# Kernel tuning notes

Measured on AMD Instinct MI355X. Metric: run time of the kernel, lower is better.

## Reference

```python
import jax, jax.numpy as jnp
import numpy as np
from jax import lax

DN = ('NCHW', 'OIHW', 'NCHW')

def _conv(x, w, b):
    # stride-2 conv, kernel 4, padding 1 (PyTorch Conv2d semantics)
    y = lax.conv_general_dilated(x, w, (2, 2), [(1, 1), (1, 1)], dimension_numbers=DN)
    return y + b[None, :, None, None]

def _deconv(x, w, b):
    # PyTorch ConvTranspose2d(k=4, stride=2, padding=1): conv with lhs_dilation=2,
    # padding k-1-p=2, kernel rot180 with in/out axes swapped ([I,O,H,W] -> [O,I,H,W])
    k = jnp.transpose(jnp.flip(w, (2, 3)), (1, 0, 2, 3))
    y = lax.conv_general_dilated(x, k, (1, 1), [(2, 2), (2, 2)], lhs_dilation=(2, 2),
                                 dimension_numbers=DN)
    return y + b[None, :, None, None]

def setup_inputs() -> dict:
    key = jax.random.key(0)
    ks = jax.random.split(key, 16)
    K, D = 1024, 2048
    s = lambda *sh: 0.05
    inp = {
        'x': jax.random.uniform(ks[0], (8, 3, 256, 256), jnp.float32),
        'enc_w1': jax.random.normal(ks[1], (128, 3, 4, 4), jnp.float32) * 0.05,
        'enc_b1': jnp.zeros((128,), jnp.float32),
        'enc_w2': jax.random.normal(ks[2], (128, 128, 4, 4), jnp.float32) * 0.02,
        'enc_b2': jnp.zeros((128,), jnp.float32),
        'enc_w3': jax.random.normal(ks[3], (D, 128, 4, 4), jnp.float32) * 0.02,
        'enc_b3': jnp.zeros((D,), jnp.float32),
        'codebook': jax.random.uniform(ks[4], (K, D), jnp.float32, -1.0 / K, 1.0 / K),
        'dec_w1': jax.random.normal(ks[5], (D, 128, 4, 4), jnp.float32) * 0.02,  # [in,out,kH,kW]
        'dec_b1': jnp.zeros((128,), jnp.float32),
        'dec_w2': jax.random.normal(ks[6], (128, 128, 4, 4), jnp.float32) * 0.02,
        'dec_b2': jnp.zeros((128,), jnp.float32),
        'dec_w3': jax.random.normal(ks[7], (128, 1, 4, 4), jnp.float32) * 0.05,
        'dec_b3': jnp.zeros((1,), jnp.float32),
    }
    return inp

def reference(x, enc_w1, enc_b1, enc_w2, enc_b2, enc_w3, enc_b3, codebook,
              dec_w1, dec_b1, dec_w2, dec_b2, dec_w3, dec_b3):
    # encoder
    h = jax.nn.relu(_conv(x, enc_w1, enc_b1))
    h = jax.nn.relu(_conv(h, enc_w2, enc_b2))
    z_e = _conv(h, enc_w3, enc_b3)                       # [B, D, H8, W8]
    B, D, Hq, Wq = z_e.shape
    z_flat = z_e.reshape(B, D, Hq * Wq).transpose(0, 2, 1)  # [B, N, D]
    # squared distances to codebook [K, D]
    dists = (jnp.sum(z_flat ** 2, axis=2, keepdims=True)
             + jnp.sum(codebook ** 2, axis=1)
             - 2.0 * jnp.einsum('bnd,kd->bnk', z_flat, codebook))  # [B, N, K]
    idx = jnp.argmin(dists, axis=2)                      # [B, N]
    z_q = codebook[idx]                                  # [B, N, D]
    z_q = z_q.transpose(0, 2, 1).reshape(B, D, Hq, Wq)
    # decoder
    h = jax.nn.relu(_deconv(z_q, dec_w1, dec_b1))
    h = jax.nn.relu(_deconv(h, dec_w2, dec_b2))
    x_recon = jax.nn.sigmoid(_deconv(h, dec_w3, dec_b3))  # [B, 1, H, W]
    sg = lax.stop_gradient
    commitment = 0.25 * jnp.mean((sg(z_e) - z_q) ** 2)
    quantization = jnp.mean((z_e - sg(z_q)) ** 2)
    return x_recon, commitment + quantization
```

## Files before the change

### kernel.cpp

```cpp
#include <hip/hip_runtime.h>

typedef __attribute__((ext_vector_type(8))) short bf16x8;
typedef __attribute__((ext_vector_type(4))) float f32x4;

__device__ __forceinline__ unsigned short f2bf(float f) {
  unsigned u = __float_as_uint(f);
  u += 0x7fff + ((u >> 16) & 1);
  return (unsigned short)(u >> 16);
}
__device__ __forceinline__ float bf2f(unsigned short h) {
  return __uint_as_float(((unsigned)h) << 16);
}

__device__ __forceinline__ void gload_lds16(const void* g, void* l) {
  __builtin_amdgcn_global_load_lds((const __attribute__((address_space(1))) void*)g,
                                   (__attribute__((address_space(3))) void*)l, 16, 0, 0);
}

__device__ __forceinline__ void pbar() {
  asm volatile("" ::: "memory");
  __builtin_amdgcn_sched_barrier(0);
  __builtin_amdgcn_s_barrier();
  __builtin_amdgcn_sched_barrier(0);
  asm volatile("" ::: "memory");
}


__global__ __launch_bounds__(256) void pack_conv_w(const float* __restrict__ w,
                                                   unsigned short* __restrict__ bt,
                                                   int Cin, int total) {
  int i = blockIdx.x * 256 + threadIdx.x;
  if (i >= total) return;
  int ci = i % Cin;
  int kk = (i / Cin) % 16;
  int co = i / (Cin * 16);
  bt[i] = f2bf(w[(size_t)co * Cin * 16 + (size_t)ci * 16 + kk]);
}

__global__ __launch_bounds__(256) void pack_deconv_w(const float* __restrict__ w,
                                                     unsigned short* __restrict__ btd,
                                                     int Cin, int total) {
  int i = blockIdx.x * 256 + threadIdx.x;
  if (i >= total) return;
  int ci = i % Cin;
  int t = (i / Cin) & 3;
  int co = (i / (Cin * 4)) & 127;
  int z = i / (Cin * 4 * 128);
  int py = z >> 1, px = z & 1;
  int ty = t >> 1, tx = t & 1;
  int ky = 2 * ty + 1 - py, kx = 2 * tx + 1 - px;
  btd[i] = f2bf(w[(((size_t)ci * 128 + co) * 4 + ky) * 4 + kx]);
}

__global__ __launch_bounds__(256) void pack_w1v(const float* __restrict__ w,
                                                unsigned short* __restrict__ bt) {
  int i = blockIdx.x * 256 + threadIdx.x;
  int ci = i & 2047;
  int n = i >> 11;
  int co = n & 127;
  int t = n >> 7;
  bt[i] = f2bf(w[(((size_t)ci * 128 + co) << 4) + t]);
}

__global__ __launch_bounds__(256) void pack_w3(const float* __restrict__ w3,
                                               float* __restrict__ wd) {
  int i = blockIdx.x * 256 + threadIdx.x;
  int ci = i & 127;
  int t = (i >> 7) & 3;
  int z = i >> 9;
  int py = z >> 1, px = z & 1, ty = t >> 1, tx = t & 1;
  int ky = 2 * ty + 1 - py, kx = 2 * tx + 1 - px;
  wd[i] = w3[ci * 16 + ky * 4 + kx];
}

__global__ __launch_bounds__(256) void pack_cb(const float* __restrict__ cb,
                                               unsigned short* __restrict__ cbb,
                                               float* __restrict__ cnorm) {
  int r = blockIdx.x;
  const float* src = cb + (size_t)r * 2048;
  float s = 0.f;
  for (int i = threadIdx.x; i < 2048; i += 256) {
    float v = src[i];
    cbb[(size_t)r * 2048 + i] = f2bf(v);
    s += v * v;
  }
  __shared__ float red[4];
  for (int off = 32; off > 0; off >>= 1) s += __shfl_down(s, off, 64);
  int lane = threadIdx.x & 63, wid = threadIdx.x >> 6;
  if (lane == 0) red[wid] = s;
  __syncthreads();
  if (threadIdx.x == 0) cnorm[r] = red[0] + red[1] + red[2] + red[3];
}

__global__ __launch_bounds__(256) void conv1_k(const float* __restrict__ x,
                                               const float* __restrict__ w1,
                                               const float* __restrict__ b1,
                                               unsigned short* __restrict__ h1) {
  __shared__ float sIn[3][4][258];
  int b = blockIdx.x >> 7, y = blockIdx.x & 127;
  for (int i = threadIdx.x; i < 3 * 4 * 258; i += 256) {
    int c = i / (4 * 258);
    int rr = (i / 258) % 4;
    int col = i % 258;
    int iy = 2 * y - 1 + rr;
    int ix = col - 1;
    float v = (iy >= 0 && iy < 256 && ix >= 0 && ix < 256)
                  ? x[((size_t)(b * 3 + c) * 256 + iy) * 256 + ix] : 0.f;
    sIn[c][rr][col] = v;
  }
  __syncthreads();
  int co = threadIdx.x & 127, xh = threadIdx.x >> 7;
  float w[3][4][4];
#pragma unroll
  for (int c = 0; c < 3; ++c)
#pragma unroll
    for (int ky = 0; ky < 4; ++ky)
#pragma unroll
      for (int kx = 0; kx < 4; ++kx)
        w[c][ky][kx] = w1[(((size_t)co * 3 + c) * 4 + ky) * 4 + kx];
  float bb = b1[co];
  for (int xi = 0; xi < 64; ++xi) {
    int xx = xh * 64 + xi;
    float acc = bb;
#pragma unroll
    for (int c = 0; c < 3; ++c)
#pragma unroll
      for (int ky = 0; ky < 4; ++ky)
#pragma unroll
        for (int kx = 0; kx < 4; ++kx)
          acc += sIn[c][ky][2 * xx + kx] * w[c][ky][kx];
    acc = acc > 0.f ? acc : 0.f;
    h1[((size_t)(b * 130 + y + 1) * 130 + (xx + 1)) * 128 + co] = f2bf(acc);
  }
}

#define GM_CONV 0
#define GM_DECONV 1
#define GM_FLAT 2
#define EP_PM 0
#define EP_FLATBF 1
#define EP_F32 2

struct GP {
  const unsigned short* A;
  const unsigned short* Bt;
  const float* bias;
  void* out;
  int Klen, Clog;
  int MXlog, MYlog;
  int WPin, strideBA;
  int HPo, WPo;
  int Nout;
  int BrowStride;
  int BclassStride;
  int classLog;
  int TPC;
  int outZ;
};

template <int BM, int GM, int EP, int RELU>
__global__ __launch_bounds__(256) void gemm_k(GP p) {
  constexpr int MFR = BM / 32;
  constexpr int CA = BM / 32;
  const int tid = threadIdx.x;
  const int lane = tid & 63;
  const int wid = tid >> 6;
  const int m0 = blockIdx.x * BM;
  const int n0 = blockIdx.y * 128;
  const int zAll = blockIdx.z;
  const int zc = zAll & ((1 << p.classLog) - 1);
  const int chunk = zAll >> p.classLog;
  const int py = zc >> 1, px = zc & 1;

  __shared__ __align__(16) unsigned short sA[BM * 64];
  __shared__ __align__(16) unsigned short sB[128 * 64];

  const unsigned short* Bt = p.Bt + (size_t)zc * p.BclassStride;
  const int C = 1 << p.Clog;
  const int tb = chunk * p.TPC;
  const int chunkOff = tb << p.Clog;
  const int sw = ((lane & 7) ^ (lane >> 3)) * 8;

  int rcA[CA];
#pragma unroll
  for (int i = 0; i < CA; ++i) {
    int r = (wid * CA + i) * 8 + (lane >> 3);
    int m = m0 + r;
    if (GM == GM_FLAT) {
      rcA[i] = m * p.Klen;
    } else {
      int mx = m & ((1 << p.MXlog) - 1);
      int my = (m >> p.MXlog) & ((1 << p.MYlog) - 1);
      int b = m >> (p.MXlog + p.MYlog);
      if (GM == GM_CONV)
        rcA[i] = b * p.strideBA + ((2 * my) * p.WPin + 2 * mx) * C;
      else
        rcA[i] = b * p.strideBA + ((my + 1) * p.WPin + (mx + 1)) * C;
    }
  }
  int rcB[4];
#pragma unroll
  for (int i = 0; i < 4; ++i) {
    int r = (wid * 4 + i) * 8 + (lane >> 3);
    rcB[i] = (n0 + r) * p.BrowStride;
  }

  f32x4 acc[MFR][4];
#pragma unroll
  for (int a = 0; a < MFR; ++a)
#pragma unroll
    for (int b = 0; b < 4; ++b) acc[a][b] = (f32x4){0.f, 0.f, 0.f, 0.f};

  const int nsteps = p.Klen >> 6;
  for (int ks = 0; ks < nsteps; ++ks) {
    const int k0 = ks << 6;
    int tap = 0;
    if (GM == GM_CONV) {
      int t = tb + (k0 >> p.Clog);
      tap = ((t >> 2) * p.WPin + (t & 3)) * C;
    } else if (GM == GM_DECONV) {
      int t = tb + (k0 >> p.Clog);
      int ty = t >> 1, tx = t & 1;
      tap = ((py - ty) * p.WPin + (px - tx)) * C;
    }
    const int ci0 = k0 & (C - 1);
    const int aoff = tap + ci0 + sw;
#pragma unroll
    for (int i = 0; i < CA; ++i)
      gload_lds16(p.A + rcA[i] + aoff, &sA[(wid * CA + i) * 512]);
#pragma unroll
    for (int i = 0; i < 4; ++i)
      gload_lds16(Bt + rcB[i] + chunkOff + k0 + sw, &sB[(wid * 4 + i) * 512]);
    __syncthreads();

#pragma unroll
    for (int kk = 0; kk < 2; ++kk) {
      bf16x8 af[MFR], bfv[4];
#pragma unroll
      for (int mf = 0; mf < MFR; ++mf) {
        int row = (wid >> 1) * (BM / 2) + mf * 16 + (lane & 15);
        int col = (kk * 64 + ((lane >> 4) << 4)) ^ ((row & 7) << 4);
        af[mf] = *(const bf16x8*)((const char*)sA + row * 128 + col);
      }
#pragma unroll
      for (int nf = 0; nf < 4; ++nf) {
        int row = (wid & 1) * 64 + nf * 16 + (lane & 15);
        int col = (kk * 64 + ((lane >> 4) << 4)) ^ ((row & 7) << 4);
        bfv[nf] = *(const bf16x8*)((const char*)sB + row * 128 + col);
      }
#pragma unroll
      for (int mf = 0; mf < MFR; ++mf)
#pragma unroll
        for (int nf = 0; nf < 4; ++nf)
          acc[mf][nf] = __builtin_amdgcn_mfma_f32_16x16x32_bf16(
              af[mf], bfv[nf], acc[mf][nf], 0, 0, 0);
    }
    __syncthreads();
  }

  const int wr = wid >> 1, wc = wid & 1;
#pragma unroll
  for (int mf = 0; mf < MFR; ++mf) {
#pragma unroll
    for (int j = 0; j < 4; ++j) {
      int row = m0 + wr * (BM / 2) + mf * 16 + ((lane >> 4) << 2) + j;
      int b = 0, my = 0, mx = 0;
      if (EP == EP_PM) {
        mx = row & ((1 << p.MXlog) - 1);
        my = (row >> p.MXlog) & ((1 << p.MYlog) - 1);
        b = row >> (p.MXlog + p.MYlog);
      }
#pragma unroll
      for (int nf = 0; nf < 4; ++nf) {
        int col = n0 + wc * 64 + nf * 16 + (lane & 15);
        float v = acc[mf][nf][j];
        if (EP == EP_PM || EP == EP_FLATBF) v += p.bias[col];
        if (RELU) v = v > 0.f ? v : 0.f;
        if (EP == EP_F32) {
          ((float*)p.out)[(size_t)row * p.Nout + col] = v;
        } else if (EP == EP_FLATBF) {
          ((unsigned short*)p.out)[(size_t)row * p.Nout + col] = f2bf(v);
        } else {
          int oy, ox;
          if (GM == GM_DECONV) {
            oy = 2 * my + py + 1;
            ox = 2 * mx + px + 1;
          } else {
            oy = my + 1;
            ox = mx + 1;
          }
          ((unsigned short*)p.out)[((size_t)(b * p.HPo + oy) * p.WPo + ox) * 128 + col] =
              f2bf(v);
        }
      }
    }
  }
}

struct G2 {
  const unsigned short* A;
  const unsigned short* Bt;
  const float* bias;
  unsigned short* out;
  int Klen;
  int WPin, strideBA;
  int Nout;
};

template <int GM>
__global__ __launch_bounds__(512, 2) void gemm256_k(G2 p) {
  __shared__ __align__(16) unsigned short lds[8 * 8192];
  const int tid = threadIdx.x, lane = tid & 63, wid = tid >> 6;
  const int wr = wid >> 2, wc = wid & 3;
  const int m0 = blockIdx.x * 256, n0 = blockIdx.y * 256;
  const int sw = ((lane & 7) ^ (lane >> 3)) * 8;
  const int xc0 = ((lane >> 4) ^ (lane & 7)) * 16;
  const int xc1 = (((lane >> 4) | 4) ^ (lane & 7)) * 16;

  int rcA[2][2], rcB[2][2];
#pragma unroll
  for (int h = 0; h < 2; ++h)
#pragma unroll
    for (int i = 0; i < 2; ++i) {
      int m = m0 + h * 128 + wid * 16 + i * 8 + (lane >> 3);
      if (GM == GM_CONV) {
        int mx = m & 31, my = (m >> 5) & 31, b = m >> 10;
        rcA[h][i] = b * p.strideBA + ((2 * my) * p.WPin + 2 * mx) * 128;
      } else {
        rcA[h][i] = m * p.Klen;
      }
      int n = n0 + h * 128 + wid * 16 + i * 8 + (lane >> 3);
      rcB[h][i] = n * p.Klen;
    }

  const int JMAX = p.Klen >> 4;

  auto stage = [&](int j) {
    if (j >= JMAX) return;
    const int T = j >> 2, type = j & 3, slot = j & 7;
    unsigned short* dst = &lds[slot * 8192 + wid * 1024];
    if (type < 2) {
      const int ko = (T << 6) + sw;
      gload_lds16(p.Bt + rcB[type][0] + ko, dst);
      gload_lds16(p.Bt + rcB[type][1] + ko, dst + 512);
    } else {
      int ko;
      if (GM == GM_CONV) {
        const int t = T >> 1;
        ko = ((t >> 2) * p.WPin + (t & 3)) * 128 + ((T & 1) << 6) + sw;
      } else {
        ko = (T << 6) + sw;
      }
      gload_lds16(p.A + rcA[type - 2][0] + ko, dst);
      gload_lds16(p.A + rcA[type - 2][1] + ko, dst + 512);
    }
  };

  f32x4 acc[8][4];
#pragma unroll
  for (int i = 0; i < 8; ++i)
#pragma unroll
    for (int j = 0; j < 4; ++j) acc[i][j] = (f32x4){0.f, 0.f, 0.f, 0.f};

#pragma unroll
  for (int j = 0; j < 6; ++j) stage(j);
  asm volatile("s_waitcnt vmcnt(4)" ::: "memory");
  pbar();

  const int NT = p.Klen >> 6;
  bf16x8 a[4][2], b0[2][2], b1[2][2];
  for (int t = 0; t < NT; ++t) {
    const int sb = (t & 1) << 2;
    const char* myA = (const char*)&lds[(sb + 2 + wr) * 8192];
    const char* myB = (const char*)&lds[(sb + (wc >> 1)) * 8192];
    const int p4 = t << 2;
#pragma unroll
    for (int mf = 0; mf < 4; ++mf) {
      const int r = mf * 16 + (lane & 15);
      a[mf][0] = *(const bf16x8*)(myA + r * 128 + xc0);
      a[mf][1] = *(const bf16x8*)(myA + r * 128 + xc1);
    }
#pragma unroll
    for (int nf = 0; nf < 2; ++nf) {
      const int c = (wc & 1) * 64 + nf * 16 + (lane & 15);
      b0[nf][0] = *(const bf16x8*)(myB + c * 128 + xc0);
      b0[nf][1] = *(const bf16x8*)(myB + c * 128 + xc1);
    }
    stage(p4 + 6);
    pbar();
    __builtin_amdgcn_s_setprio(1);
#pragma unroll
    for (int mf = 0; mf < 4; ++mf)
#pragma unroll
      for (int nf = 0; nf < 2; ++nf)
#pragma unroll
        for (int kk = 0; kk < 2; ++kk)
          acc[mf][nf] = __builtin_amdgcn_mfma_f32_16x16x32_bf16(
              a[mf][kk], b0[nf][kk], acc[mf][nf], 0, 0, 0);
    __builtin_amdgcn_s_setprio(0);
    pbar();
#pragma unroll
    for (int nf = 0; nf < 2; ++nf) {
      const int c = (wc & 1) * 64 + (nf + 2) * 16 + (lane & 15);
      b1[nf][0] = *(const bf16x8*)(myB + c * 128 + xc0);
      b1[nf][1] = *(const bf16x8*)(myB + c * 128 + xc1);
    }
    stage(p4 + 7);
    pbar();
    __builtin_amdgcn_s_setprio(1);
#pragma unroll
    for (int mf = 0; mf < 4; ++mf)
#pragma unroll
      for (int nf = 0; nf < 2; ++nf)
#pragma unroll
        for (int kk = 0; kk < 2; ++kk)
          acc[mf][nf + 2] = __builtin_amdgcn_mfma_f32_16x16x32_bf16(
              a[mf][kk], b1[nf][kk], acc[mf][nf + 2], 0, 0, 0);
    __builtin_amdgcn_s_setprio(0);
    pbar();
#pragma unroll
    for (int mf = 0; mf < 4; ++mf) {
      const int r = 64 + mf * 16 + (lane & 15);
      a[mf][0] = *(const bf16x8*)(myA + r * 128 + xc0);
      a[mf][1] = *(const bf16x8*)(myA + r * 128 + xc1);
    }
    stage(p4 + 8);
    pbar();
    __builtin_amdgcn_s_setprio(1);
#pragma unroll
    for (int mf = 0; mf < 4; ++mf)
#pragma unroll
      for (int nf = 0; nf < 2; ++nf)
#pragma unroll
        for (int kk = 0; kk < 2; ++kk)
          acc[mf + 4][nf + 2] = __builtin_amdgcn_mfma_f32_16x16x32_bf16(
              a[mf][kk], b1[nf][kk], acc[mf + 4][nf + 2], 0, 0, 0);
    __builtin_amdgcn_s_setprio(0);
    pbar();
    stage(p4 + 9);
    pbar();
    __builtin_amdgcn_s_setprio(1);
#pragma unroll
    for (int mf = 0; mf < 4; ++mf)
#pragma unroll
      for (int nf = 0; nf < 2; ++nf)
#pragma unroll
        for (int kk = 0; kk < 2; ++kk)
          acc[mf + 4][nf] = __builtin_amdgcn_mfma_f32_16x16x32_bf16(
              a[mf][kk], b0[nf][kk], acc[mf + 4][nf], 0, 0, 0);
    __builtin_amdgcn_s_setprio(0);
    asm volatile("s_waitcnt vmcnt(4)" ::: "memory");
    pbar();
  }

#pragma unroll
  for (int mf = 0; mf < 8; ++mf) {
#pragma unroll
    for (int j = 0; j < 4; ++j) {
      int row = m0 + wr * 128 + mf * 16 + ((lane >> 4) << 2) + j;
#pragma unroll
      for (int nf = 0; nf < 4; ++nf) {
        int col = n0 + wc * 64 + nf * 16 + (lane & 15);
        float v = acc[mf][nf][j] + p.bias[col];
        p.out[(size_t)row * p.Nout + col] = f2bf(v);
      }
    }
  }
}

struct GV {
  const unsigned short* A;
  const unsigned short* Bt;
  const float* cnorm;
  float* cval;
  int* cidx;
};

__global__ __launch_bounds__(512, 2) void vq8_k(GV p) {
  __shared__ __align__(16) unsigned short lds[49152];
  const int tid = threadIdx.x, lane = tid & 63, wid = tid >> 6;
  const int wr = wid >> 2, wc = wid & 3;
  const int m0 = blockIdx.x * 128, n0 = blockIdx.y * 256;
  const int sw = ((lane & 7) ^ (lane >> 3)) * 8;
  const int xc0 = ((lane >> 4) ^ (lane & 7)) * 16;
  const int xc1 = (((lane >> 4) | 4) ^ (lane & 7)) * 16;
  const int K = 2048;

  int rcA[2];
#pragma unroll
  for (int h = 0; h < 2; ++h)
    rcA[h] = (m0 + h * 64 + wid * 8 + (lane >> 3)) * K;
  int rcB[2][2];
#pragma unroll
  for (int h = 0; h < 2; ++h)
#pragma unroll
    for (int i = 0; i < 2; ++i)
      rcB[h][i] = (n0 + h * 128 + wid * 16 + i * 8 + (lane >> 3)) * K;

  auto stage = [&](int j) {
    if (j >= 128) return;
    const int T = j >> 2, type = j & 3;
    unsigned short* reg = &lds[(T & 1) * 24576];
    const int ko = (T << 6) + sw;
    if (type < 2) {
      gload_lds16(p.A + rcA[type] + ko, reg + type * 4096 + wid * 512);
    } else {
      unsigned short* d = reg + 8192 + (type - 2) * 8192 + wid * 1024;
      gload_lds16(p.Bt + rcB[type - 2][0] + ko, d);
      gload_lds16(p.Bt + rcB[type - 2][1] + ko, d + 512);
    }
  };

  f32x4 acc[4][4];
#pragma unroll
  for (int i = 0; i < 4; ++i)
#pragma unroll
    for (int j = 0; j < 4; ++j) acc[i][j] = (f32x4){0.f, 0.f, 0.f, 0.f};

#pragma unroll
  for (int j = 0; j < 6; ++j) stage(j);
  asm volatile("s_waitcnt vmcnt(2)" ::: "memory");
  pbar();

  bf16x8 a[4][2], b[4][2];
  for (int t = 0; t < 32; ++t) {
    const char* reg = (const char*)&lds[(t & 1) * 24576];
    const char* myA = reg + wr * 8192;
    const char* myB = reg + 16384 + (wc >> 1) * 16384;
    const int p4 = t << 2;
#pragma unroll
    for (int mf = 0; mf < 4; ++mf) {
      const int r = mf * 16 + (lane & 15);
      a[mf][0] = *(const bf16x8*)(myA + r * 128 + xc0);
      a[mf][1] = *(const bf16x8*)(myA + r * 128 + xc1);
    }
#pragma unroll
    for (int nf = 0; nf < 4; ++nf) {
      const int c = (wc & 1) * 64 + nf * 16 + (lane & 15);
      b[nf][0] = *(const bf16x8*)(myB + c * 128 + xc0);
      b[nf][1] = *(const bf16x8*)(myB + c * 128 + xc1);
    }
    stage(p4 + 6);
    stage(p4 + 7);
    pbar();
    __builtin_amdgcn_s_setprio(1);
#pragma unroll
    for (int mf = 0; mf < 4; ++mf)
#pragma unroll
      for (int nf = 0; nf < 2; ++nf)
#pragma unroll
        for (int kk = 0; kk < 2; ++kk)
          acc[mf][nf] = __builtin_amdgcn_mfma_f32_16x16x32_bf16(
              a[mf][kk], b[nf][kk], acc[mf][nf], 0, 0, 0);
    __builtin_amdgcn_s_setprio(0);
    pbar();
    stage(p4 + 8);
    stage(p4 + 9);
    pbar();
    __builtin_amdgcn_s_setprio(1);
#pragma unroll
    for (int mf = 0; mf < 4; ++mf)
#pragma unroll
      for (int nf = 2; nf < 4; ++nf)
#pragma unroll
        for (int kk = 0; kk < 2; ++kk)
          acc[mf][nf] = __builtin_amdgcn_mfma_f32_16x16x32_bf16(
              a[mf][kk], b[nf][kk], acc[mf][nf], 0, 0, 0);
    __builtin_amdgcn_s_setprio(0);
    asm volatile("s_waitcnt vmcnt(2)" ::: "memory");
    pbar();
  }

  __syncthreads();
  float* sV = (float*)lds;
  int* sI = (int*)(sV + 512);
  float cn[4];
#pragma unroll
  for (int nf = 0; nf < 4; ++nf)
    cn[nf] = p.cnorm[n0 + wc * 64 + nf * 16 + (lane & 15)];
#pragma unroll
  for (int mf = 0; mf < 4; ++mf) {
#pragma unroll
    for (int j = 0; j < 4; ++j) {
      float bv = 3.4e38f;
      int bi = 0x7fffffff;
#pragma unroll
      for (int nf = 0; nf < 4; ++nf) {
        int col = n0 + wc * 64 + nf * 16 + (lane & 15);
        float d = cn[nf] - 2.f * acc[mf][nf][j];
        if (d < bv) { bv = d; bi = col; }
      }
#pragma unroll
      for (int w = 1; w <= 8; w <<= 1) {
        float ov = __shfl_xor(bv, w, 64);
        int oi = __shfl_xor(bi, w, 64);
        if (ov < bv || (ov == bv && oi < bi)) { bv = ov; bi = oi; }
      }
      int lrow = wr * 64 + mf * 16 + ((lane >> 4) << 2) + j;
      if ((lane & 15) == 0) { sV[lrow * 4 + wc] = bv; sI[lrow * 4 + wc] = bi; }
    }
  }
  __syncthreads();
  if (tid < 128) {
    float bv = sV[tid * 4];
    int bi = sI[tid * 4];
#pragma unroll
    for (int c = 1; c < 4; ++c) {
      float v = sV[tid * 4 + c];
      int i2 = sI[tid * 4 + c];
      if (v < bv) { bv = v; bi = i2; }
    }
    p.cval[(size_t)(m0 + tid) * 4 + blockIdx.y] = bv;
    p.cidx[(size_t)(m0 + tid) * 4 + blockIdx.y] = bi;
  }
}


__global__ __launch_bounds__(256) void argfin_k(const float* __restrict__ cval,
                                                const int* __restrict__ cidx,
                                                int* __restrict__ idx,
                                                float* __restrict__ dmin) {
  int m = blockIdx.x * 256 + threadIdx.x;
  float bv = cval[(size_t)m * 4];
  int bi = cidx[(size_t)m * 4];
#pragma unroll
  for (int j = 1; j < 4; ++j) {
    float v = cval[(size_t)m * 4 + j];
    int i2 = cidx[(size_t)m * 4 + j];
    if (v < bv) { bv = v; bi = i2; }
  }
  idx[m] = bi;
  dmin[m] = bv;
}


__global__ __launch_bounds__(256) void lossz_k(const unsigned short* __restrict__ zf,
                                               const float* __restrict__ dmin,
                                               float* __restrict__ part) {
  int m = blockIdx.x;
  int tid = threadIdx.x;
  bf16x8 av = ((const bf16x8*)(zf + (size_t)m * 2048))[tid];
  float s = 0.f;
#pragma unroll
  for (int i = 0; i < 8; ++i) {
    float z = bf2f((unsigned short)av[i]);
    s += z * z;
  }
  __shared__ float red[4];
  for (int off = 32; off > 0; off >>= 1) s += __shfl_down(s, off, 64);
  int lane = tid & 63, wid = tid >> 6;
  if (lane == 0) red[wid] = s;
  __syncthreads();
  if (tid == 0) part[m] = red[0] + red[1] + red[2] + red[3] + dmin[m];
}

__global__ __launch_bounds__(256) void loss_final_k(const float* __restrict__ part,
                                                    float* __restrict__ out) {
  int tid = threadIdx.x;
  float s = 0.f;
  for (int i = tid; i < 8192; i += 256) s += part[i];
  __shared__ float red[4];
  for (int off = 32; off > 0; off >>= 1) s += __shfl_down(s, off, 64);
  if ((tid & 63) == 0) red[tid >> 6] = s;
  __syncthreads();
  if (tid == 0) out[0] = 1.25f * (red[0] + red[1] + red[2] + red[3]) / 16777216.f;
}

__global__ __launch_bounds__(256) void dc1gather_k(const float* __restrict__ V,
                                                   const int* __restrict__ idx,
                                                   const float* __restrict__ bias,
                                                   unsigned short* __restrict__ h3) {
  int b = blockIdx.x >> 6;
  int oy = blockIdx.x & 63;
  int co = threadIdx.x & 127;
  int xh = threadIdx.x >> 7;
  __shared__ int sIdx[2][32];
  int iyA = (oy + 1) >> 1, kyA = (oy + 1) & 1;
  int iyB = iyA - 1, kyB = kyA + 2;
  if (threadIdx.x < 64) {
    int which = threadIdx.x >> 5;
    int ix = threadIdx.x & 31;
    int iy = which ? iyB : iyA;
    sIdx[which][ix] = (iy >= 0 && iy < 32) ? idx[(b << 10) + (iy << 5) + ix] : -1;
  }
  __syncthreads();
  float bb = bias[co];
  for (int xi = 0; xi < 32; ++xi) {
    int ox = xh * 32 + xi;
    int ixA = (ox + 1) >> 1, kxA = (ox + 1) & 1;
    int ixB = ixA - 1, kxB = kxA + 2;
    float s = bb;
    int kAA = (ixA < 32) ? sIdx[0][ixA] : -1;
    if (kAA >= 0) s += V[((size_t)(kAA * 16 + kyA * 4 + kxA)) * 128 + co];
    int kAB = (ixB >= 0) ? sIdx[0][ixB] : -1;
    if (kAB >= 0) s += V[((size_t)(kAB * 16 + kyA * 4 + kxB)) * 128 + co];
    int kBA = (ixA < 32) ? sIdx[1][ixA] : -1;
    if (kBA >= 0) s += V[((size_t)(kBA * 16 + kyB * 4 + kxA)) * 128 + co];
    int kBB = (ixB >= 0) ? sIdx[1][ixB] : -1;
    if (kBB >= 0) s += V[((size_t)(kBB * 16 + kyB * 4 + kxB)) * 128 + co];
    s = s > 0.f ? s : 0.f;
    h3[((size_t)(b * 66 + oy + 1) * 66 + (ox + 1)) * 128 + co] = f2bf(s);
  }
}

__global__ __launch_bounds__(256) void deconv3_k(const unsigned short* __restrict__ h4,
                                                 const float* __restrict__ wd,
                                                 const float* __restrict__ b3,
                                                 float* __restrict__ out) {
  __shared__ __align__(16) char sRow[2 * 130 * 272];
  __shared__ float sW[2048];
  const int tid = threadIdx.x;
  const int b = blockIdx.x >> 8, oy = blockIdx.x & 255;
  const int py = oy & 1, uy = oy >> 1;
  const int g0 = uy + py;
  for (int i = tid; i < 2048; i += 256) sW[i] = wd[i];
  for (int g = tid; g < 4160; g += 256) {
    int r = (g >= 2080) ? 1 : 0;
    int gg = g - r * 2080;
    int px = gg >> 4, k = gg & 15;
    const bf16x8* src =
        (const bf16x8*)(h4 + (((size_t)(b * 130 + g0 + r) * 130 + px) << 7) + k * 8);
    *(bf16x8*)(sRow + r * 35360 + px * 272 + k * 16) = *src;
  }
  __syncthreads();
  const int ox = tid;
  const int pxp = ox & 1, ux = ox >> 1;
  const int z = py * 2 + pxp;
  float s = b3[0];
#pragma unroll
  for (int ty = 0; ty < 2; ++ty) {
#pragma unroll
    for (int tx = 0; tx < 2; ++tx) {
      int ixp = ux + 1 + pxp - tx;
      const char* base = sRow + (1 - ty) * 35360 + ixp * 272;
      const float* wp = &sW[z * 512 + (ty * 2 + tx) * 128];
#pragma unroll
      for (int k = 0; k < 16; ++k) {
        bf16x8 v = *(const bf16x8*)(base + k * 16);
#pragma unroll
        for (int i = 0; i < 8; ++i)
          s += bf2f((unsigned short)v[i]) * wp[k * 8 + i];
      }
    }
  }
  out[(size_t)blockIdx.x * 256 + ox] = 1.f / (1.f + __expf(-s));
}

extern "C" void kernel_launch(void* const* d_in, const int* in_sizes, int n_in,
                              void* d_out, int out_size, void* d_ws, size_t ws_size,
                              hipStream_t stream) {
  const float* x = (const float*)d_in[0];
  const float* ew1 = (const float*)d_in[1];
  const float* eb1 = (const float*)d_in[2];
  const float* ew2 = (const float*)d_in[3];
  const float* eb2 = (const float*)d_in[4];
  const float* ew3 = (const float*)d_in[5];
  const float* eb3 = (const float*)d_in[6];
  const float* cb = (const float*)d_in[7];
  const float* dw1 = (const float*)d_in[8];
  const float* db1 = (const float*)d_in[9];
  const float* dw2 = (const float*)d_in[10];
  const float* db2 = (const float*)d_in[11];
  const float* dw3 = (const float*)d_in[12];
  const float* db3 = (const float*)d_in[13];
  float* out = (float*)d_out;

  char* w = (char*)d_ws;
  size_t off = 0;
  auto alloc = [&](size_t bytes) {
    char* p = w + off;
    off = (off + bytes + 255) & ~(size_t)255;
    return p;
  };
  const size_t sz_h1 = 8ull * 130 * 130 * 128 * 2;
  const size_t sz_h2 = 8ull * 66 * 66 * 128 * 2;
  const size_t sz_zf = 8192ull * 2048 * 2;
  unsigned short* h1 = (unsigned short*)alloc(sz_h1);
  unsigned short* h2 = (unsigned short*)alloc(sz_h2);
  unsigned short* zf = (unsigned short*)alloc(sz_zf);
  unsigned short* cbb = (unsigned short*)alloc(1024ull * 2048 * 2);
  float* cnorm = (float*)alloc(1024 * 4);
  int* idx = (int*)alloc(8192 * 4);
  unsigned short* h4 = (unsigned short*)alloc(sz_h1);
  unsigned short* bt2 = (unsigned short*)alloc(128ull * 2048 * 2);
  unsigned short* bt3 = (unsigned short*)alloc(2048ull * 2048 * 2);
  unsigned short* btw1 = (unsigned short*)alloc(2048ull * 2048 * 2);
  unsigned short* btd2 = (unsigned short*)alloc(4ull * 128 * 512 * 2);
  float* V = (float*)alloc(1024ull * 16 * 128 * 4);
  float* lpart = (float*)alloc(8192 * 4);
  float* wd3 = (float*)alloc(2048 * 4);
  unsigned short* h3 = (unsigned short*)alloc(sz_h2);
  float* cval = (float*)alloc(8192ull * 4 * 4);
  int* cidx = (int*)alloc(8192ull * 4 * 4);
  float* dmin = (float*)alloc(8192 * 4);

  hipMemsetAsync(h1, 0, sz_h1, stream);
  hipMemsetAsync(h2, 0, sz_h2, stream);
  hipMemsetAsync(h3, 0, sz_h2, stream);
  hipMemsetAsync(h4, 0, sz_h1, stream);

  pack_conv_w<<<(128 * 128 * 16) / 256, 256, 0, stream>>>(ew2, bt2, 128, 128 * 128 * 16);
  pack_conv_w<<<(2048 * 128 * 16) / 256, 256, 0, stream>>>(ew3, bt3, 128, 2048 * 128 * 16);
  pack_w1v<<<(2048 * 2048) / 256, 256, 0, stream>>>(dw1, btw1);
  pack_deconv_w<<<(4 * 128 * 4 * 128) / 256, 256, 0, stream>>>(dw2, btd2, 128, 4 * 128 * 4 * 128);
  pack_w3<<<8, 256, 0, stream>>>(dw3, wd3);
  pack_cb<<<1024, 256, 0, stream>>>(cb, cbb, cnorm);
  conv1_k<<<1024, 256, 0, stream>>>(x, ew1, eb1, h1);

  GP pcw = {cbb, btw1, nullptr, V, 2048, 11, 0, 0, 0, 0, 0, 0,
            2048, 2048, 0, 0, 0, 0};
  gemm_k<64, GM_FLAT, EP_F32, 0><<<dim3(16, 16, 1), 256, 0, stream>>>(pcw);

  GP p2 = {h1, bt2, eb2, h2, 2048, 7, 6, 6, 130, 130 * 130 * 128, 66, 66,
           128, 2048, 0, 0, 0, 0};
  gemm_k<64, GM_CONV, EP_PM, 1><<<dim3(512, 1, 1), 256, 0, stream>>>(p2);

  G2 g3 = {h2, bt3, eb3, zf, 2048, 66, 66 * 66 * 128, 2048};
  gemm256_k<GM_CONV><<<dim3(32, 8, 1), 512, 0, stream>>>(g3);

  GV pv = {zf, cbb, cnorm, cval, cidx};
  vq8_k<<<dim3(64, 4, 1), 512, 0, stream>>>(pv);
  argfin_k<<<32, 256, 0, stream>>>(cval, cidx, idx, dmin);

  lossz_k<<<8192, 256, 0, stream>>>(zf, dmin, lpart);
  loss_final_k<<<1, 256, 0, stream>>>(lpart, out + 524288);

  dc1gather_k<<<512, 256, 0, stream>>>(V, idx, db1, h3);

  GP pd2 = {h3, btd2, db2, h4, 512, 7, 6, 6, 66, 66 * 66 * 128, 130, 130,
            128, 512, 128 * 512, 2, 0, 0};
  gemm_k<128, GM_DECONV, EP_PM, 1><<<dim3(256, 1, 4), 256, 0, stream>>>(pd2);

  deconv3_k<<<2048, 256, 0, stream>>>(h4, wd3, db3, out);
  (void)in_sizes; (void)n_in; (void)out_size; (void)ws_size;
}
```

Measured before the change: 417.0 us.

## Merge packing kernels, zero only halos, fuse argmin into loss, deepen GEMM prefetch

Replaces four full-buffer memsets of the padded activation buffers with a kernel that zeroes only the one-pixel halo border. It merges five weight-packing launches into one kernel and folds the final argmin reduction into the loss kernel, dropping a launch and the dmin buffer. It also deepens the GEMM software pipeline by one stage, with the vmcnt waits adjusted to match. The aim is to cut launch overhead and memset bandwidth, at the risk of more in-flight LDS stages and an incorrect halo if the interiors are not fully overwritten.

```diff
diff --git a/kernel.cpp b/kernel.cpp
--- a/kernel.cpp
+++ b/kernel.cpp
@@ -25,52 +25,69 @@
   asm volatile("" ::: "memory");
 }
 
-
-__global__ __launch_bounds__(256) void pack_conv_w(const float* __restrict__ w,
-                                                   unsigned short* __restrict__ bt,
-                                                   int Cin, int total) {
+__global__ __launch_bounds__(256) void halo_k(unsigned short* __restrict__ h1,
+                                              unsigned short* __restrict__ h2,
+                                              unsigned short* __restrict__ h3,
+                                              unsigned short* __restrict__ h4) {
+  int pid = blockIdx.x * 2 + (threadIdx.x >> 7);
+  int co = threadIdx.x & 127;
+  unsigned short* buf;
+  int b, e, SP;
+  if (pid < 8256) {
+    buf = (pid < 4128) ? h1 : h4;
+    int rel = (pid < 4128) ? pid : pid - 4128;
+    b = rel / 516; e = rel % 516; SP = 130;
+    int y, x;
+    if (e < 130) { y = 0; x = e; }
+    else if (e < 260) { y = 129; x = e - 130; }
+    else if (e < 388) { y = 1 + (e - 260); x = 0; }
+    else { y = 1 + (e - 388); x = 129; }
+    buf[(((size_t)(b * SP + y)) * SP + x) * 128 + co] = 0;
+  } else {
+    buf = (pid < 10336) ? h2 : h3;
+    int rel = pid - ((pid < 10336) ? 8256 : 10336);
+    b = rel / 260; e = rel % 260; SP = 66;
+    int y, x;
+    if (e < 66) { y = 0; x = e; }
+    else if (e < 132) { y = 65; x = e - 66; }
+    else if (e < 196) { y = 1 + (e - 132); x = 0; }
+    else { y = 1 + (e - 196); x = 65; }
+    buf[(((size_t)(b * SP + y)) * SP + x) * 128 + co] = 0;
+  }
+}
+
+__global__ __launch_bounds__(256) void megapack_k(
+    const float* __restrict__ ew2, const float* __restrict__ ew3,
+    const float* __restrict__ dw1, const float* __restrict__ dw2,
+    const float* __restrict__ dw3, unsigned short* __restrict__ bt2,
+    unsigned short* __restrict__ bt3, unsigned short* __restrict__ btw1,
+    unsigned short* __restrict__ btd2, float* __restrict__ wd3) {
   int i = blockIdx.x * 256 + threadIdx.x;
-  if (i >= total) return;
-  int ci = i % Cin;
-  int kk = (i / Cin) % 16;
-  int co = i / (Cin * 16);
-  bt[i] = f2bf(w[(size_t)co * Cin * 16 + (size_t)ci * 16 + kk]);
-}
-
-__global__ __launch_bounds__(256) void pack_deconv_w(const float* __restrict__ w,
-                                                     unsigned short* __restrict__ btd,
-                                                     int Cin, int total) {
-  int i = blockIdx.x * 256 + threadIdx.x;
-  if (i >= total) return;
-  int ci = i % Cin;
-  int t = (i / Cin) & 3;
-  int co = (i / (Cin * 4)) & 127;
-  int z = i / (Cin * 4 * 128);
-  int py = z >> 1, px = z & 1;
-  int ty = t >> 1, tx = t & 1;
-  int ky = 2 * ty + 1 - py, kx = 2 * tx + 1 - px;
-  btd[i] = f2bf(w[(((size_t)ci * 128 + co) * 4 + ky) * 4 + kx]);
-}
-
-__global__ __launch_bounds__(256) void pack_w1v(const float* __restrict__ w,
-                                                unsigned short* __restrict__ bt) {
-  int i = blockIdx.x * 256 + threadIdx.x;
-  int ci = i & 2047;
-  int n = i >> 11;
-  int co = n & 127;
-  int t = n >> 7;
-  bt[i] = f2bf(w[(((size_t)ci * 128 + co) << 4) + t]);
-}
-
-__global__ __launch_bounds__(256) void pack_w3(const float* __restrict__ w3,
-                                               float* __restrict__ wd) {
-  int i = blockIdx.x * 256 + threadIdx.x;
-  int ci = i & 127;
-  int t = (i >> 7) & 3;
-  int z = i >> 9;
-  int py = z >> 1, px = z & 1, ty = t >> 1, tx = t & 1;
-  int ky = 2 * ty + 1 - py, kx = 2 * tx + 1 - px;
-  wd[i] = w3[ci * 16 + ky * 4 + kx];
+  if (i < 262144) {
+    int ci = i & 127, kk = (i >> 7) & 15, co = i >> 11;
+    bt2[i] = f2bf(ew2[(size_t)co * 2048 + ci * 16 + kk]);
+  } else if (i < 4456448) {
+    int j = i - 262144;
+    int ci = j & 127, kk = (j >> 7) & 15, co = j >> 11;
+    bt3[j] = f2bf(ew3[(size_t)co * 2048 + ci * 16 + kk]);
+  } else if (i < 8650752) {
+    int j = i - 4456448;
+    int ci = j & 2047, n = j >> 11;
+    int co = n & 127, t = n >> 7;
+    btw1[j] = f2bf(dw1[(((size_t)ci * 128 + co) << 4) + t]);
+  } else if (i < 8912896) {
+    int j = i - 8650752;
+    int ci = j & 127, t = (j >> 7) & 3, co = (j >> 9) & 127, z = j >> 16;
+    int py = z >> 1, px = z & 1, ty = t >> 1, tx = t & 1;
+    int ky = 2 * ty + 1 - py, kx = 2 * tx + 1 - px;
+    btd2[j] = f2bf(dw2[(((size_t)ci * 128 + co) * 4 + ky) * 4 + kx]);
+  } else {
+    int j = i - 8912896;
+    int ci = j & 127, t = (j >> 7) & 3, z = j >> 9;
+    int py = z >> 1, px = z & 1, ty = t >> 1, tx = t & 1;
+    int ky = 2 * ty + 1 - py, kx = 2 * tx + 1 - px;
+    wd3[j] = dw3[ci * 16 + ky * 4 + kx];
+  }
 }
 
 __global__ __launch_bounds__(256) void pack_cb(const float* __restrict__ cb,
@@ -363,8 +380,8 @@
     for (int j = 0; j < 4; ++j) acc[i][j] = (f32x4){0.f, 0.f, 0.f, 0.f};
 
 #pragma unroll
-  for (int j = 0; j < 6; ++j) stage(j);
-  asm volatile("s_waitcnt vmcnt(4)" ::: "memory");
+  for (int j = 0; j < 7; ++j) stage(j);
+  asm volatile("s_waitcnt vmcnt(6)" ::: "memory");
   pbar();
 
   const int NT = p.Klen >> 6;
@@ -386,7 +403,7 @@
       b0[nf][0] = *(const bf16x8*)(myB + c * 128 + xc0);
       b0[nf][1] = *(const bf16x8*)(myB + c * 128 + xc1);
     }
-    stage(p4 + 6);
+    stage(p4 + 7);
     pbar();
     __builtin_amdgcn_s_setprio(1);
 #pragma unroll
@@ -405,7 +422,7 @@
       b1[nf][0] = *(const bf16x8*)(myB + c * 128 + xc0);
       b1[nf][1] = *(const bf16x8*)(myB + c * 128 + xc1);
     }
-    stage(p4 + 7);
+    stage(p4 + 8);
     pbar();
     __builtin_amdgcn_s_setprio(1);
 #pragma unroll
@@ -424,7 +441,7 @@
       a[mf][0] = *(const bf16x8*)(myA + r * 128 + xc0);
       a[mf][1] = *(const bf16x8*)(myA + r * 128 + xc1);
     }
-    stage(p4 + 8);
+    stage(p4 + 9);
     pbar();
     __builtin_amdgcn_s_setprio(1);
 #pragma unroll
@@ -437,7 +454,7 @@
               a[mf][kk], b1[nf][kk], acc[mf + 4][nf + 2], 0, 0, 0);
     __builtin_amdgcn_s_setprio(0);
     pbar();
-    stage(p4 + 9);
+    stage(p4 + 10);
     pbar();
     __builtin_amdgcn_s_setprio(1);
 #pragma unroll
@@ -449,7 +466,7 @@
           acc[mf + 4][nf] = __builtin_amdgcn_mfma_f32_16x16x32_bf16(
               a[mf][kk], b0[nf][kk], acc[mf + 4][nf], 0, 0, 0);
     __builtin_amdgcn_s_setprio(0);
-    asm volatile("s_waitcnt vmcnt(4)" ::: "memory");
+    asm volatile("s_waitcnt vmcnt(6)" ::: "memory");
     pbar();
   }
 
@@ -615,28 +632,11 @@
   }
 }
 
-
-__global__ __launch_bounds__(256) void argfin_k(const float* __restrict__ cval,
+__global__ __launch_bounds__(256) void lossz2_k(const unsigned short* __restrict__ zf,
+                                                const float* __restrict__ cval,
                                                 const int* __restrict__ cidx,
                                                 int* __restrict__ idx,
-                                                float* __restrict__ dmin) {
-  int m = blockIdx.x * 256 + threadIdx.x;
-  float bv = cval[(size_t)m * 4];
-  int bi = cidx[(size_t)m * 4];
-#pragma unroll
-  for (int j = 1; j < 4; ++j) {
-    float v = cval[(size_t)m * 4 + j];
-    int i2 = cidx[(size_t)m * 4 + j];
-    if (v < bv) { bv = v; bi = i2; }
-  }
-  idx[m] = bi;
-  dmin[m] = bv;
-}
-
-
-__global__ __launch_bounds__(256) void lossz_k(const unsigned short* __restrict__ zf,
-                                               const float* __restrict__ dmin,
-                                               float* __restrict__ part) {
+                                                float* __restrict__ part) {
   int m = blockIdx.x;
   int tid = threadIdx.x;
   bf16x8 av = ((const bf16x8*)(zf + (size_t)m * 2048))[tid];
@@ -651,7 +651,18 @@
   int lane = tid & 63, wid = tid >> 6;
   if (lane == 0) red[wid] = s;
   __syncthreads();
-  if (tid == 0) part[m] = red[0] + red[1] + red[2] + red[3] + dmin[m];
+  if (tid == 0) {
+    float bv = cval[(size_t)m * 4];
+    int bi = cidx[(size_t)m * 4];
+#pragma unroll
+    for (int j = 1; j < 4; ++j) {
+      float v = cval[(size_t)m * 4 + j];
+      int i2 = cidx[(size_t)m * 4 + j];
+      if (v < bv) { bv = v; bi = i2; }
+    }
+    idx[m] = bi;
+    part[m] = red[0] + red[1] + red[2] + red[3] + bv;
+  }
 }
 
 __global__ __launch_bounds__(256) void loss_final_k(const float* __restrict__ part,
@@ -792,18 +803,10 @@
   unsigned short* h3 = (unsigned short*)alloc(sz_h2);
   float* cval = (float*)alloc(8192ull * 4 * 4);
   int* cidx = (int*)alloc(8192ull * 4 * 4);
-  float* dmin = (float*)alloc(8192 * 4);
-
-  hipMemsetAsync(h1, 0, sz_h1, stream);
-  hipMemsetAsync(h2, 0, sz_h2, stream);
-  hipMemsetAsync(h3, 0, sz_h2, stream);
-  hipMemsetAsync(h4, 0, sz_h1, stream);
-
-  pack_conv_w<<<(128 * 128 * 16) / 256, 256, 0, stream>>>(ew2, bt2, 128, 128 * 128 * 16);
-  pack_conv_w<<<(2048 * 128 * 16) / 256, 256, 0, stream>>>(ew3, bt3, 128, 2048 * 128 * 16);
-  pack_w1v<<<(2048 * 2048) / 256, 256, 0, stream>>>(dw1, btw1);
-  pack_deconv_w<<<(4 * 128 * 4 * 128) / 256, 256, 0, stream>>>(dw2, btd2, 128, 4 * 128 * 4 * 128);
-  pack_w3<<<8, 256, 0, stream>>>(dw3, wd3);
+
+  halo_k<<<6208, 256, 0, stream>>>(h1, h2, h3, h4);
+  megapack_k<<<34824, 256, 0, stream>>>(ew2, ew3, dw1, dw2, dw3,
+                                        bt2, bt3, btw1, btd2, wd3);
   pack_cb<<<1024, 256, 0, stream>>>(cb, cbb, cnorm);
   conv1_k<<<1024, 256, 0, stream>>>(x, ew1, eb1, h1);
 
@@ -820,9 +823,8 @@
 
   GV pv = {zf, cbb, cnorm, cval, cidx};
   vq8_k<<<dim3(64, 4, 1), 512, 0, stream>>>(pv);
-  argfin_k<<<32, 256, 0, stream>>>(cval, cidx, idx, dmin);
-
-  lossz_k<<<8192, 256, 0, stream>>>(zf, dmin, lpart);
+
+  lossz2_k<<<8192, 256, 0, stream>>>(zf, cval, cidx, idx, lpart);
   loss_final_k<<<1, 256, 0, stream>>>(lpart, out + 524288);
 
   dc1gather_k<<<512, 256, 0, stream>>>(V, idx, db1, h3);
```

Result: faster. 386.7 us (-7.3%).
